# Performance work log

Hardware: AMD Instinct MI355X
Metric: run time of the kernel (lower is better)

## Reference

```python
import jax, jax.numpy as jnp
import numpy as np

NEG_BIG = -1e16  # matches the torch module's mask multiplier (fits in fp32)


def setup_inputs() -> dict:
    key = jax.random.key(0)
    k1, k2, k3, k4 = jax.random.split(key, 4)
    B, S, T, D, O = 8, 2048, 2048, 1024, 1024
    src = jax.random.normal(k1, (B, S, D), dtype=jnp.float32)
    tgt = jax.random.normal(k2, (B, T, D), dtype=jnp.float32)
    mask = jax.random.randint(k3, (T, B, S), 0, 2, dtype=jnp.int32)
    W = jax.random.normal(k4, (O, 2 * D), dtype=jnp.float32) * (1.0 / np.sqrt(2 * D))
    b = jnp.zeros((O,), dtype=jnp.float32)
    return {"src": src, "tgt": tgt, "mask": mask, "W": W, "b": b}


def reference(src, tgt, mask, W, b):
    # scores: [B, T, S] = tgt @ src^T
    weight = jnp.einsum('btd,bsd->bts', tgt, src)
    # mask [T,B,S] -> [B,T,S], additive large-negative where mask==1
    weight = weight + mask.transpose(1, 0, 2).astype(weight.dtype) * NEG_BIG
    # NOTE: original softmax is over dim=1 (the tgt axis), faithful here
    weight = jax.nn.softmax(weight, axis=1)
    weight_sum = jnp.einsum('bts,bsd->btd', weight, src)  # [B,T,D]
    cat = jnp.concatenate([weight_sum, tgt], axis=2)      # [B,T,2D]
    output = cat @ W.T + b                                 # [B,T,O]
    return output, weight
```

## Files before the change

kernel.cpp:

```cpp
#include <hip/hip_runtime.h>

#define Bb 8
#define Ss 2048
#define Tt 2048
#define Dd 1024
#define Oo 1024
#define NEG_BIG -1.0e16f

typedef unsigned short u16;
typedef __attribute__((ext_vector_type(4))) float f32x4;
typedef __attribute__((ext_vector_type(8))) _Float16 f16x8;
typedef __attribute__((ext_vector_type(8))) u16 u16x8;
typedef __attribute__((ext_vector_type(4))) u16 u16x4;

__device__ __forceinline__ u16 f2h(float x) {
  return __builtin_bit_cast(u16, (_Float16)x);
}

__device__ __forceinline__ void gload_lds16(const void* g, void* l) {
  __builtin_amdgcn_global_load_lds(
      (__attribute__((address_space(1))) void*)const_cast<void*>(g),
      (__attribute__((address_space(3))) void*)l, 16, 0, 0);
}

__device__ __forceinline__ f16x8 ldfrag(const u16* p) {
  return __builtin_bit_cast(f16x8, *(const u16x8*)p);
}

__global__ __launch_bounds__(256) void cvt_f16(const float* __restrict__ in,
                                               u16* __restrict__ out16) {
  const size_t i = ((size_t)blockIdx.x * 256 + threadIdx.x) * 4;
  float4 v = *(const float4*)(in + i);
  u16x4 h = {f2h(v.x), f2h(v.y), f2h(v.z), f2h(v.w)};
  *(u16x4*)(out16 + i) = h;
}

__global__ __launch_bounds__(256) void prep_src(const float* __restrict__ src,
                                                u16* __restrict__ src16,
                                                u16* __restrict__ srcT) {
  __shared__ u16 tile[64][72];
  const int b = blockIdx.z;
  const int d0 = blockIdx.x * 64;
  const int s0 = blockIdx.y * 64;
  const int tid = threadIdx.x;
  const int sl = tid >> 4;
  const int dl = (tid & 15) * 4;
#pragma unroll
  for (int p = 0; p < 4; ++p) {
    const int srow = s0 + sl + p * 16;
    float4 v = *(const float4*)(src + ((size_t)b * Ss + srow) * Dd + d0 + dl);
    u16 h0 = f2h(v.x), h1 = f2h(v.y), h2 = f2h(v.z), h3 = f2h(v.w);
    *(u16x4*)(src16 + ((size_t)b * Ss + srow) * Dd + d0 + dl) = (u16x4){h0, h1, h2, h3};
    tile[dl + 0][sl + p * 16] = h0;
    tile[dl + 1][sl + p * 16] = h1;
    tile[dl + 2][sl + p * 16] = h2;
    tile[dl + 3][sl + p * 16] = h3;
  }
  __syncthreads();
  const int dl2 = tid >> 4;
  const int sl2 = (tid & 15) * 4;
#pragma unroll
  for (int p = 0; p < 4; ++p) {
    const int drow = d0 + dl2 + p * 16;
    u16x4 vv = {tile[dl2 + p * 16][sl2], tile[dl2 + p * 16][sl2 + 1],
                tile[dl2 + p * 16][sl2 + 2], tile[dl2 + p * 16][sl2 + 3]};
    *(u16x4*)(srcT + ((size_t)b * Dd + drow) * Ss + s0 + sl2) = vv;
  }
}

template <int MODE>
__global__ __launch_bounds__(512, 2) void gemm256(
    const u16* __restrict__ A, size_t ldA, size_t sA,
    const u16* __restrict__ A2,
    const u16* __restrict__ Bm, size_t ldB, size_t sB,
    int NT,
    float* __restrict__ outF, u16* __restrict__ outH,
    const int* __restrict__ mask, const float* __restrict__ bias) {
  __shared__ __align__(16) u16 sh[66560];
  const int b = blockIdx.z;
  const int tn = blockIdx.x, tm = blockIdx.y;
  const int tid = threadIdx.x;
  const int w = tid >> 6, l = tid & 63;
  const int wr = w >> 2, wc = w & 3;

  const int sr0 = w * 16 + (l >> 3);
  const int scb = (((l & 7) ^ (l >> 3)) << 4);
  const int fc0 = (((l >> 4) * 16) ^ ((l & 7) << 4)) >> 1;
  const int fc1 = ((64 + (l >> 4) * 16) ^ ((l & 7) << 4)) >> 1;

  auto STAGE = [&](int isB, int ds, int hh, int ts) {
    int dst = (isB ? 32768 : 0) + ds * 16384 + hh * 8192 + w * 1024;
    if (ts >= NT) { ts = NT - 1; dst = 65536; }
    const u16* srcBase;
    size_t ld;
    int rowBase;
    int kbyte = ts * 128;
    if (isB) {
      srcBase = Bm + (size_t)b * sB;
      ld = ldB;
      rowBase = tn * 256 + hh * 128;
    } else {
      if constexpr (MODE == 2) {
        srcBase = (ts < 16 ? A : A2) + (size_t)b * sA;
        kbyte = (ts & 15) * 128;
      } else {
        srcBase = A + (size_t)b * sA;
      }
      ld = ldA;
      rowBase = tm * 256 + hh * 128;
    }
    const char* s0 = (const char*)srcBase + (size_t)(rowBase + sr0) * (ld * 2) + kbyte + scb;
    const char* s1 = (const char*)srcBase + (size_t)(rowBase + sr0 + 8) * (ld * 2) + kbyte + scb;
    gload_lds16(s0, &sh[dst]);
    gload_lds16(s1, &sh[dst + 512]);
  };

  f32x4 acc[8][4];
#pragma unroll
  for (int m = 0; m < 8; ++m)
#pragma unroll
    for (int n = 0; n < 4; ++n) acc[m][n] = (f32x4){0.f, 0.f, 0.f, 0.f};
  f16x8 bf[4][2], af[2][2];

  STAGE(1, 0, 0, 0);
  STAGE(1, 0, 1, 0);
  STAGE(0, 0, 0, 0);
  STAGE(0, 0, 1, 0);
  STAGE(1, 1, 0, 1);
  STAGE(1, 1, 1, 1);
  asm volatile("s_waitcnt vmcnt(4)" ::: "memory");
  asm volatile("s_barrier" ::: "memory");

  const int NITER = NT >> 1;
  for (int it = 0; it < NITER; ++it) {
#pragma unroll
    for (int p = 0; p < 8; ++p) {
      const int q = p & 3, d = (p >> 2) & 1;
      if (q == 0) {
#pragma unroll
        for (int ni = 0; ni < 4; ++ni) {
          const int rb = wc * 64 + ni * 16 + (l & 15);
          bf[ni][0] = ldfrag(&sh[32768 + d * 16384 + rb * 64 + fc0]);
          bf[ni][1] = ldfrag(&sh[32768 + d * 16384 + rb * 64 + fc1]);
        }
      }
#pragma unroll
      for (int mi = 0; mi < 2; ++mi) {
        const int ra = wr * 128 + q * 32 + mi * 16 + (l & 15);
        af[mi][0] = ldfrag(&sh[d * 16384 + ra * 64 + fc0]);
        af[mi][1] = ldfrag(&sh[d * 16384 + ra * 64 + fc1]);
      }
      {
        const int j = 8 * it + p + 6;
        const int ts = j >> 2, sub = j & 3;
        STAGE(sub < 2, ts & 1, sub & 1, ts);
      }
      if (q == 3) asm volatile("s_waitcnt vmcnt(4)" ::: "memory");
      asm volatile("s_barrier" ::: "memory");
      __builtin_amdgcn_s_setprio(1);
#pragma unroll
      for (int mi = 0; mi < 2; ++mi)
#pragma unroll
        for (int ni = 0; ni < 4; ++ni) {
          acc[2 * q + mi][ni] = __builtin_amdgcn_mfma_f32_16x16x32_f16(
              af[mi][0], bf[ni][0], acc[2 * q + mi][ni], 0, 0, 0);
          acc[2 * q + mi][ni] = __builtin_amdgcn_mfma_f32_16x16x32_f16(
              af[mi][1], bf[ni][1], acc[2 * q + mi][ni], 0, 0, 0);
        }
      __builtin_amdgcn_s_setprio(0);
      asm volatile("s_barrier" ::: "memory");
    }
  }

  const int fr = l & 15, fq = l >> 4;
  const int r0 = tm * 256 + wr * 128;
  const int c0 = tn * 256 + wc * 64;
#pragma unroll
  for (int m = 0; m < 8; ++m) {
#pragma unroll
    for (int n = 0; n < 4; ++n) {
#pragma unroll
      for (int j = 0; j < 4; ++j) {
        const int r = r0 + m * 16 + fq * 4 + j;
        const int c = c0 + n * 16 + fr;
        float v = acc[m][n][j];
        if constexpr (MODE == 0) {
          const int mk = mask[((size_t)r * Bb + b) * Ss + c];
          v += (float)mk * NEG_BIG;
          outF[((size_t)b * Tt + r) * Ss + c] = v;
        } else if constexpr (MODE == 1) {
          outH[((size_t)b * Tt + r) * Dd + c] = f2h(v);
        } else {
          outF[((size_t)b * Tt + r) * Oo + c] = v + bias[c];
        }
      }
    }
  }
}

__global__ __launch_bounds__(256) void colstats(const float* __restrict__ sc,
                                                float* __restrict__ mcol,
                                                float* __restrict__ rlcol) {
  const int b = blockIdx.y;
  const int c = threadIdx.x & 31;
  const int seg = threadIdx.x >> 5;
  const int s = blockIdx.x * 32 + c;
  const float* p = sc + ((size_t)b * Tt + seg * 256) * Ss + s;
  float m = -3.0e38f, lsum = 0.0f;
#pragma unroll 4
  for (int i = 0; i < 256; ++i) {
    float v = p[(size_t)i * Ss];
    float mn = fmaxf(m, v);
    lsum = lsum * __expf(m - mn) + __expf(v - mn);
    m = mn;
  }
  __shared__ float sm[8][32], sl[8][32];
  sm[seg][c] = m;
  sl[seg][c] = lsum;
  __syncthreads();
  if (seg == 0) {
    float M = sm[0][c];
#pragma unroll
    for (int k = 1; k < 8; ++k) M = fmaxf(M, sm[k][c]);
    float L = 0.0f;
#pragma unroll
    for (int k = 0; k < 8; ++k) L += sl[k][c] * __expf(sm[k][c] - M);
    mcol[(size_t)b * Ss + s] = M;
    rlcol[(size_t)b * Ss + s] = 1.0f / L;
  }
}

__global__ __launch_bounds__(256) void normalize(float* __restrict__ sc,
                                                 const float* __restrict__ mcol,
                                                 const float* __restrict__ rlcol,
                                                 u16* __restrict__ w16) {
  const size_t i = ((size_t)blockIdx.x * 256 + threadIdx.x) * 4;
  const int s = (int)(i & (Ss - 1));
  const size_t bt = i >> 11;
  const int b = (int)(bt >> 11);
  float4 v = *(const float4*)(sc + i);
  float4 m4 = *(const float4*)(mcol + (size_t)b * Ss + s);
  float4 r4 = *(const float4*)(rlcol + (size_t)b * Ss + s);
  float w0 = __expf(v.x - m4.x) * r4.x;
  float w1 = __expf(v.y - m4.y) * r4.y;
  float w2 = __expf(v.z - m4.z) * r4.z;
  float w3 = __expf(v.w - m4.w) * r4.w;
  *(float4*)(sc + i) = make_float4(w0, w1, w2, w3);
  *(u16x4*)(w16 + i) = (u16x4){f2h(w0), f2h(w1), f2h(w2), f2h(w3)};
}

extern "C" void kernel_launch(void* const* d_in, const int* in_sizes, int n_in,
                              void* d_out, int out_size, void* d_ws, size_t ws_size,
                              hipStream_t stream) {
  const float* src = (const float*)d_in[0];
  const float* tgt = (const float*)d_in[1];
  const int* mask = (const int*)d_in[2];
  const float* W = (const float*)d_in[3];
  const float* bias = (const float*)d_in[4];
  float* out = (float*)d_out;
  float* scores = out + (size_t)Bb * Tt * Oo;

  u16* tgt16 = (u16*)d_ws;
  u16* src16 = tgt16 + (size_t)Bb * Tt * Dd;
  u16* srcT = src16 + (size_t)Bb * Ss * Dd;
  u16* wsum16 = srcT + (size_t)Bb * Dd * Ss;
  u16* w16 = wsum16 + (size_t)Bb * Tt * Dd;
  u16* W16 = w16 + (size_t)Bb * Tt * Ss;
  float* mcol = (float*)(W16 + (size_t)Oo * 2 * Dd);
  float* rlcol = mcol + (size_t)Bb * Ss;

  cvt_f16<<<(Bb * Tt * Dd) / 1024, 256, 0, stream>>>(tgt, tgt16);
  cvt_f16<<<(Oo * 2 * Dd) / 1024, 256, 0, stream>>>(W, W16);
  prep_src<<<dim3(Dd / 64, Ss / 64, Bb), 256, 0, stream>>>(src, src16, srcT);

  gemm256<0><<<dim3(Ss / 256, Tt / 256, Bb), 512, 0, stream>>>(
      tgt16, (size_t)Dd, (size_t)Tt * Dd, nullptr,
      src16, (size_t)Dd, (size_t)Ss * Dd, Dd / 64,
      scores, nullptr, mask, nullptr);

  colstats<<<dim3(Ss / 32, Bb), 256, 0, stream>>>(scores, mcol, rlcol);
  normalize<<<(size_t)(Bb * Tt) * Ss / 1024, 256, 0, stream>>>(scores, mcol, rlcol, w16);

  gemm256<1><<<dim3(Dd / 256, Tt / 256, Bb), 512, 0, stream>>>(
      w16, (size_t)Ss, (size_t)Tt * Ss, nullptr,
      srcT, (size_t)Ss, (size_t)Dd * Ss, Ss / 64,
      nullptr, wsum16, nullptr, nullptr);

  gemm256<2><<<dim3(Oo / 256, Tt / 256, Bb), 512, 0, stream>>>(
      wsum16, (size_t)Dd, (size_t)Tt * Dd, tgt16,
      W16, (size_t)2 * Dd, (size_t)0, 2 * Dd / 64,
      out, nullptr, nullptr, bias);
}
```

Before: 686.0 us.

## Pack mask into bitfield and apply it in softmax stats and normalize

Adds a pre-pass that packs the int32 [T,B,S] mask into 32-bit words in [B,T,S] order, stored in the wsum16 workspace before that buffer is reused. The score GEMM epilogue no longer does strided int32 mask reads; instead colstats and normalize read the compact bits and add the large negative themselves. colstats is widened to 64 columns and 512 threads, and the GEMM drops its occupancy hint of 2 in launch bounds. The goal is to cut mask traffic and uncoalesced epilogue loads, at the cost of one extra full pass over the mask plus some bit work in two kernels.

```diff
diff --git a/kernel.cpp b/kernel.cpp
--- a/kernel.cpp
+++ b/kernel.cpp
@@ -8,6 +8,7 @@
 #define NEG_BIG -1.0e16f
 
 typedef unsigned short u16;
+typedef unsigned int u32;
 typedef __attribute__((ext_vector_type(4))) float f32x4;
 typedef __attribute__((ext_vector_type(8))) _Float16 f16x8;
 typedef __attribute__((ext_vector_type(8))) u16 u16x8;
@@ -33,6 +34,25 @@
   float4 v = *(const float4*)(in + i);
   u16x4 h = {f2h(v.x), f2h(v.y), f2h(v.z), f2h(v.w)};
   *(u16x4*)(out16 + i) = h;
+}
+
+__global__ __launch_bounds__(256) void pack_mask(const int* __restrict__ mask,
+                                                 u32* __restrict__ bits) {
+  const size_t widx = (size_t)blockIdx.x * 256 + threadIdx.x;
+  const int sw = (int)(widx & (Ss / 32 - 1));
+  const int t = (int)((widx >> 6) & (Tt - 1));
+  const int b = (int)(widx >> 17);
+  const int* p = mask + ((size_t)t * Bb + b) * Ss + sw * 32;
+  u32 w = 0;
+#pragma unroll
+  for (int q = 0; q < 8; ++q) {
+    int4 v = *(const int4*)(p + q * 4);
+    w |= (u32)((v.x != 0) ? 1u : 0u) << (q * 4 + 0);
+    w |= (u32)((v.y != 0) ? 1u : 0u) << (q * 4 + 1);
+    w |= (u32)((v.z != 0) ? 1u : 0u) << (q * 4 + 2);
+    w |= (u32)((v.w != 0) ? 1u : 0u) << (q * 4 + 3);
+  }
+  bits[widx] = w;
 }
 
 __global__ __launch_bounds__(256) void prep_src(const float* __restrict__ src,
@@ -69,13 +89,13 @@
 }
 
 template <int MODE>
-__global__ __launch_bounds__(512, 2) void gemm256(
+__global__ __launch_bounds__(512) void gemm256(
     const u16* __restrict__ A, size_t ldA, size_t sA,
     const u16* __restrict__ A2,
     const u16* __restrict__ Bm, size_t ldB, size_t sB,
     int NT,
     float* __restrict__ outF, u16* __restrict__ outH,
-    const int* __restrict__ mask, const float* __restrict__ bias) {
+    const float* __restrict__ bias) {
   __shared__ __align__(16) u16 sh[66560];
   const int b = blockIdx.z;
   const int tn = blockIdx.x, tm = blockIdx.y;
@@ -185,8 +205,6 @@
         const int c = c0 + n * 16 + fr;
         float v = acc[m][n][j];
         if constexpr (MODE == 0) {
-          const int mk = mask[((size_t)r * Bb + b) * Ss + c];
-          v += (float)mk * NEG_BIG;
           outF[((size_t)b * Tt + r) * Ss + c] = v;
         } else if constexpr (MODE == 1) {
           outH[((size_t)b * Tt + r) * Dd + c] = f2h(v);
@@ -198,23 +216,27 @@
   }
 }
 
-__global__ __launch_bounds__(256) void colstats(const float* __restrict__ sc,
+__global__ __launch_bounds__(512) void colstats(const float* __restrict__ sc,
+                                                const u32* __restrict__ bits,
                                                 float* __restrict__ mcol,
                                                 float* __restrict__ rlcol) {
   const int b = blockIdx.y;
-  const int c = threadIdx.x & 31;
-  const int seg = threadIdx.x >> 5;
-  const int s = blockIdx.x * 32 + c;
-  const float* p = sc + ((size_t)b * Tt + seg * 256) * Ss + s;
+  const int c = threadIdx.x & 63;
+  const int seg = threadIdx.x >> 6;
+  const int s = blockIdx.x * 64 + c;
+  const int sh5 = s & 31;
   float m = -3.0e38f, lsum = 0.0f;
 #pragma unroll 4
   for (int i = 0; i < 256; ++i) {
-    float v = p[(size_t)i * Ss];
+    const size_t idx = ((size_t)b * Tt + seg * 256 + i) * Ss + s;
+    float v = sc[idx];
+    const u32 wbits = bits[idx >> 5];
+    v += (float)((wbits >> sh5) & 1u) * NEG_BIG;
     float mn = fmaxf(m, v);
     lsum = lsum * __expf(m - mn) + __expf(v - mn);
     m = mn;
   }
-  __shared__ float sm[8][32], sl[8][32];
+  __shared__ float sm[8][64], sl[8][64];
   sm[seg][c] = m;
   sl[seg][c] = lsum;
   __syncthreads();
@@ -231,20 +253,26 @@
 }
 
 __global__ __launch_bounds__(256) void normalize(float* __restrict__ sc,
+                                                 const u32* __restrict__ bits,
                                                  const float* __restrict__ mcol,
                                                  const float* __restrict__ rlcol,
                                                  u16* __restrict__ w16) {
   const size_t i = ((size_t)blockIdx.x * 256 + threadIdx.x) * 4;
   const int s = (int)(i & (Ss - 1));
-  const size_t bt = i >> 11;
-  const int b = (int)(bt >> 11);
+  const int b = (int)(i >> 22);
+  const u32 wbits = bits[i >> 5];
+  const int sh5 = s & 31;
   float4 v = *(const float4*)(sc + i);
   float4 m4 = *(const float4*)(mcol + (size_t)b * Ss + s);
   float4 r4 = *(const float4*)(rlcol + (size_t)b * Ss + s);
-  float w0 = __expf(v.x - m4.x) * r4.x;
-  float w1 = __expf(v.y - m4.y) * r4.y;
-  float w2 = __expf(v.z - m4.z) * r4.z;
-  float w3 = __expf(v.w - m4.w) * r4.w;
+  float v0 = v.x + (float)((wbits >> (sh5 + 0)) & 1u) * NEG_BIG;
+  float v1 = v.y + (float)((wbits >> (sh5 + 1)) & 1u) * NEG_BIG;
+  float v2 = v.z + (float)((wbits >> (sh5 + 2)) & 1u) * NEG_BIG;
+  float v3 = v.w + (float)((wbits >> (sh5 + 3)) & 1u) * NEG_BIG;
+  float w0 = __expf(v0 - m4.x) * r4.x;
+  float w1 = __expf(v1 - m4.y) * r4.y;
+  float w2 = __expf(v2 - m4.z) * r4.z;
+  float w3 = __expf(v3 - m4.w) * r4.w;
   *(float4*)(sc + i) = make_float4(w0, w1, w2, w3);
   *(u16x4*)(w16 + i) = (u16x4){f2h(w0), f2h(w1), f2h(w2), f2h(w3)};
 }
@@ -268,7 +296,9 @@
   u16* W16 = w16 + (size_t)Bb * Tt * Ss;
   float* mcol = (float*)(W16 + (size_t)Oo * 2 * Dd);
   float* rlcol = mcol + (size_t)Bb * Ss;
-
+  u32* bits = (u32*)wsum16;
+
+  pack_mask<<<(Bb * Tt * (Ss / 32)) / 256, 256, 0, stream>>>(mask, bits);
   cvt_f16<<<(Bb * Tt * Dd) / 1024, 256, 0, stream>>>(tgt, tgt16);
   cvt_f16<<<(Oo * 2 * Dd) / 1024, 256, 0, stream>>>(W, W16);
   prep_src<<<dim3(Dd / 64, Ss / 64, Bb), 256, 0, stream>>>(src, src16, srcT);
@@ -276,18 +306,18 @@
   gemm256<0><<<dim3(Ss / 256, Tt / 256, Bb), 512, 0, stream>>>(
       tgt16, (size_t)Dd, (size_t)Tt * Dd, nullptr,
       src16, (size_t)Dd, (size_t)Ss * Dd, Dd / 64,
-      scores, nullptr, mask, nullptr);
-
-  colstats<<<dim3(Ss / 32, Bb), 256, 0, stream>>>(scores, mcol, rlcol);
-  normalize<<<(size_t)(Bb * Tt) * Ss / 1024, 256, 0, stream>>>(scores, mcol, rlcol, w16);
+      scores, nullptr, nullptr);
+
+  colstats<<<dim3(Ss / 64, Bb), 512, 0, stream>>>(scores, bits, mcol, rlcol);
+  normalize<<<(size_t)(Bb * Tt) * Ss / 1024, 256, 0, stream>>>(scores, bits, mcol, rlcol, w16);
 
   gemm256<1><<<dim3(Dd / 256, Tt / 256, Bb), 512, 0, stream>>>(
       w16, (size_t)Ss, (size_t)Tt * Ss, nullptr,
       srcT, (size_t)Ss, (size_t)Dd * Ss, Ss / 64,
-      nullptr, wsum16, nullptr, nullptr);
+      nullptr, wsum16, nullptr);
 
   gemm256<2><<<dim3(Oo / 256, Tt / 256, Bb), 512, 0, stream>>>(
       wsum16, (size_t)Dd, (size_t)Tt * Dd, tgt16,
       W16, (size_t)2 * Dd, (size_t)0, 2 * Dd / 64,
-      out, nullptr, nullptr, bias);
-}
+      out, nullptr, bias);
+}
```

New measurement: 668.1 us. -2.6%, faster.
